# Kernel tuning notes

Measured on AMD Instinct MI355X. Metric: run time of the kernel, lower is better.

Reference implementation:

```python
import jax, jax.numpy as jnp
import numpy as np

N = 50000      # nodes
E = 800000     # edges (before self loops)
D_IN = 256
D_H = 256
D_OUT = 64     # num_classes
SLOPE = 0.01   # leaky_relu slope


def setup_inputs() -> dict:
    key = jax.random.key(0)
    ks = jax.random.split(key, 8)
    x = jax.random.normal(ks[0], (N, D_IN), dtype=jnp.float32)
    edge_index = jax.random.randint(ks[1], (2, E), 0, N, dtype=jnp.int32)
    s = 0.05
    W1 = jax.random.normal(ks[2], (D_H, D_IN), dtype=jnp.float32) * s
    b1 = jnp.zeros((D_H,), dtype=jnp.float32)
    W2 = jax.random.normal(ks[3], (D_H, D_H), dtype=jnp.float32) * s
    b2 = jnp.zeros((D_H,), dtype=jnp.float32)
    W3 = jax.random.normal(ks[4], (D_OUT, D_H), dtype=jnp.float32) * s
    b3 = jnp.zeros((D_OUT,), dtype=jnp.float32)
    return {"x": x, "edge_index": edge_index, "W1": W1, "b1": b1,
            "W2": W2, "b2": b2, "W3": W3, "b3": b3}


def _gcn_layer(x, W, b, src, dst):
    # PyG GCNConv: h = x @ W^T; out[dst] += d^{-1/2}[src] d^{-1/2}[dst] * h[src]; out += b
    h = x @ W.T                                             # [N, out]
    ones = jnp.ones(src.shape[0], dtype=h.dtype)
    deg = jax.ops.segment_sum(ones, dst, num_segments=N)    # includes self loops
    dinv = jnp.where(deg > 0, jax.lax.rsqrt(deg), 0.0)
    norm = dinv[src] * dinv[dst]                            # [E+N]
    msg = h[src] * norm[:, None]                            # gather + scale
    out = jax.ops.segment_sum(msg, dst, num_segments=N)     # scatter-add
    return out + b


def reference(x, edge_index, W1, b1, W2, b2, W3, b3):
    src, dst = edge_index[0], edge_index[1]
    loop = jnp.arange(N, dtype=src.dtype)                   # add self loops
    src = jnp.concatenate([src, loop])
    dst = jnp.concatenate([dst, loop])
    act = lambda h: jax.nn.leaky_relu(h, negative_slope=SLOPE)
    h1 = act(_gcn_layer(x, W1, b1, src, dst))
    h2 = act(_gcn_layer(h1, W2, b2, src, dst))
    logits = _gcn_layer(h2, W3, b3, src, dst)               # no activation on last layer
    return (h1, h2, logits)
```

## Files before the change

kernel.cpp:

```cpp
#include <hip/hip_runtime.h>

#define N_NODES 50000
#define E_EDGES 800000
#define SLOPE 0.01f

typedef __attribute__((ext_vector_type(8))) short bf16x8;
typedef __attribute__((ext_vector_type(4))) float floatx4;

__device__ __forceinline__ unsigned short f2bf(float f) {
    unsigned u = __builtin_bit_cast(unsigned, f);
    unsigned r = (u + 0x7FFFu + ((u >> 16) & 1u)) >> 16;
    return (unsigned short)r;
}
__device__ __forceinline__ float bf2f(unsigned short h) {
    unsigned u = ((unsigned)h) << 16;
    return __builtin_bit_cast(float, u);
}


__global__ void f32_to_bf16_kernel(const float* __restrict__ in,
                                   unsigned short* __restrict__ out, int n4) {
    int i = blockIdx.x * blockDim.x + threadIdx.x;
    if (i < n4) {
        float4 v = ((const float4*)in)[i];
        ushort4 o;
        o.x = f2bf(v.x); o.y = f2bf(v.y); o.z = f2bf(v.z); o.w = f2bf(v.w);
        ((ushort4*)out)[i] = o;
    }
}

__global__ void wfrag_kernel(const float* __restrict__ Wf,
                             unsigned short* __restrict__ out, int n4) {
    int idx = blockIdx.x * blockDim.x + threadIdx.x;
    if (idx >= n4) return;
    int n = idx >> 6;
    int k = (idx & 63) << 2;
    float4 v = ((const float4*)Wf)[idx];
    int jt = n >> 4, lm = n & 15, kk = k >> 5, q = (k >> 3) & 3, e = k & 7;
    int off = ((jt * 8 + kk) * 64 + q * 16 + lm) * 8 + e;
    ushort4 o;
    o.x = f2bf(v.x); o.y = f2bf(v.y); o.z = f2bf(v.z); o.w = f2bf(v.w);
    *(ushort4*)(out + off) = o;
}


__global__ void zero_counts_kernel(int* __restrict__ counts) {
    int i = blockIdx.x * blockDim.x + threadIdx.x;
    if (i < N_NODES) counts[i] = 0;
}

__global__ void hist_kernel(const int* __restrict__ dst, int* __restrict__ counts) {
    int e = blockIdx.x * blockDim.x + threadIdx.x;
    if (e < E_EDGES) atomicAdd(&counts[dst[e]], 1);
}

__global__ void dinv_kernel(const int* __restrict__ counts, float* __restrict__ dinv) {
    int i = blockIdx.x * blockDim.x + threadIdx.x;
    if (i < N_NODES) dinv[i] = rsqrtf((float)(counts[i] + 1));
}

#define SB 1024
__global__ __launch_bounds__(SB) void scan1_kernel(const int* __restrict__ counts,
                                                   int* __restrict__ partial,
                                                   int* __restrict__ bsum) {
    __shared__ int wsum[16];
    int tid = threadIdx.x, lane = tid & 63, wid = tid >> 6;
    int i = blockIdx.x * SB + tid;
    int v = (i < N_NODES) ? counts[i] : 0;
    int x = v;
    #pragma unroll
    for (int off = 1; off < 64; off <<= 1) {
        int y = __shfl_up(x, off, 64);
        if (lane >= off) x += y;
    }
    if (lane == 63) wsum[wid] = x;
    __syncthreads();
    if (wid == 0) {
        int s = (lane < 16) ? wsum[lane] : 0;
        #pragma unroll
        for (int off = 1; off < 16; off <<= 1) {
            int y = __shfl_up(s, off, 64);
            if (lane >= off) s += y;
        }
        if (lane < 16) wsum[lane] = s;
    }
    __syncthreads();
    int woff = wid ? wsum[wid - 1] : 0;
    if (i < N_NODES) partial[i] = woff + x - v;
    if (tid == SB - 1) bsum[blockIdx.x] = woff + x;
}

__global__ void scan2_kernel(int* __restrict__ bsum, int nb) {
    int lane = threadIdx.x;
    int v = (lane < nb) ? bsum[lane] : 0;
    #pragma unroll
    for (int off = 1; off < 64; off <<= 1) {
        int y = __shfl_up(v, off, 64);
        if (lane >= off) v += y;
    }
    if (lane < nb) bsum[lane] = v;
}

__global__ void scan3_kernel(int* __restrict__ row_ptr, const int* __restrict__ bsum,
                             int* __restrict__ cursor, int nb) {
    int i = blockIdx.x * blockDim.x + threadIdx.x;
    if (i < N_NODES) {
        int c = i >> 10;
        int off = c ? bsum[c - 1] : 0;
        int ex = row_ptr[i] + off;
        row_ptr[i] = ex;
        cursor[i] = ex;
    }
    if (i == 0) row_ptr[N_NODES] = bsum[nb - 1];
}

__global__ void scatter_kernel(const int* __restrict__ src, const int* __restrict__ dst,
                               int* __restrict__ cursor, int* __restrict__ col_idx) {
    int e = blockIdx.x * blockDim.x + threadIdx.x;
    if (e < E_EDGES) {
        int pos = atomicAdd(&cursor[dst[e]], 1);
        col_idx[pos] = src[e];
    }
}


template<int WAVES_M, int WAVES_N, int MT, int NT>
__global__ __launch_bounds__(256) void gemm_frag_kernel(
        const unsigned short* __restrict__ Ab,
        const unsigned short* __restrict__ Bf,
        const float* __restrict__ dinv,
        unsigned short* __restrict__ C, int M, int Nc) {
    const int wave = threadIdx.x >> 6, lane = threadIdx.x & 63;
    const int lm = lane & 15, q = lane >> 4;
    const int bm = blockIdx.x * (WAVES_M * MT * 16);
    const int bn = blockIdx.y * (WAVES_N * NT * 16);
    const int wm = (wave / WAVES_N) * (MT * 16);
    const int wn = (wave % WAVES_N) * (NT * 16);
    const int jt0 = (bn + wn) >> 4;

    const unsigned short* arow[MT];
    #pragma unroll
    for (int i = 0; i < MT; ++i) {
        int r = bm + wm + i * 16 + lm;
        if (r >= M) r = M - 1;
        arow[i] = Ab + (size_t)r * 256 + q * 8;
    }

    floatx4 acc[MT][NT] = {};

    #pragma unroll
    for (int kk = 0; kk < 8; ++kk) {
        bf16x8 a[MT], b[NT];
        #pragma unroll
        for (int i = 0; i < MT; ++i)
            a[i] = *(const bf16x8*)(arow[i] + kk * 32);
        #pragma unroll
        for (int j = 0; j < NT; ++j)
            b[j] = *(const bf16x8*)(Bf + (((jt0 + j) * 8 + kk) * 64 + lane) * 8);
        #pragma unroll
        for (int i = 0; i < MT; ++i)
            #pragma unroll
            for (int j = 0; j < NT; ++j)
                acc[i][j] = __builtin_amdgcn_mfma_f32_16x16x32_bf16(a[i], b[j], acc[i][j], 0, 0, 0);
    }

    #pragma unroll
    for (int i = 0; i < MT; ++i) {
        int rb = bm + wm + i * 16 + q * 4;
        #pragma unroll
        for (int r = 0; r < 4; ++r) {
            int row = rb + r;
            if (row < M) {
                float dd = dinv[row];
                #pragma unroll
                for (int j = 0; j < NT; ++j)
                    C[(size_t)row * Nc + bn + wn + j * 16 + lm] = f2bf(acc[i][j][r] * dd);
            }
        }
    }
}


template<bool ACT>
__global__ __launch_bounds__(256) void agg256_kernel(
        const int* __restrict__ row_ptr, const int* __restrict__ col_idx,
        const float* __restrict__ dinv, const unsigned short* __restrict__ hs,
        const float* __restrict__ bias,
        float* __restrict__ out, unsigned short* __restrict__ outb) {
    int node = __builtin_amdgcn_readfirstlane(blockIdx.x * 4 + (threadIdx.x >> 6));
    int lane = threadIdx.x & 63;

    float dd = dinv[node];
    ushort4 sv = ((const ushort4*)(hs + (size_t)node * 256))[lane];
    float ax = bf2f(sv.x), ay = bf2f(sv.y), az = bf2f(sv.z), aw = bf2f(sv.w);

    int beg = row_ptr[node], end = row_ptr[node + 1];
    int j = beg;
    for (; j + 3 < end; j += 4) {
        int s0 = col_idx[j], s1 = col_idx[j + 1], s2 = col_idx[j + 2], s3 = col_idx[j + 3];
        ushort4 v0 = ((const ushort4*)(hs + (size_t)s0 * 256))[lane];
        ushort4 v1 = ((const ushort4*)(hs + (size_t)s1 * 256))[lane];
        ushort4 v2 = ((const ushort4*)(hs + (size_t)s2 * 256))[lane];
        ushort4 v3 = ((const ushort4*)(hs + (size_t)s3 * 256))[lane];
        ax += bf2f(v0.x); ay += bf2f(v0.y); az += bf2f(v0.z); aw += bf2f(v0.w);
        ax += bf2f(v1.x); ay += bf2f(v1.y); az += bf2f(v1.z); aw += bf2f(v1.w);
        ax += bf2f(v2.x); ay += bf2f(v2.y); az += bf2f(v2.z); aw += bf2f(v2.w);
        ax += bf2f(v3.x); ay += bf2f(v3.y); az += bf2f(v3.z); aw += bf2f(v3.w);
    }
    for (; j < end; ++j) {
        int s = col_idx[j];
        ushort4 v = ((const ushort4*)(hs + (size_t)s * 256))[lane];
        ax += bf2f(v.x); ay += bf2f(v.y); az += bf2f(v.z); aw += bf2f(v.w);
    }

    const float4 b4 = ((const float4*)bias)[lane];
    ax = fmaf(ax, dd, b4.x); ay = fmaf(ay, dd, b4.y);
    az = fmaf(az, dd, b4.z); aw = fmaf(aw, dd, b4.w);
    if (ACT) {
        ax = ax > 0.f ? ax : SLOPE * ax;
        ay = ay > 0.f ? ay : SLOPE * ay;
        az = az > 0.f ? az : SLOPE * az;
        aw = aw > 0.f ? aw : SLOPE * aw;
    }
    float4 o; o.x = ax; o.y = ay; o.z = az; o.w = aw;
    ((float4*)(out + (size_t)node * 256))[lane] = o;
    ushort4 ob; ob.x = f2bf(ax); ob.y = f2bf(ay); ob.z = f2bf(az); ob.w = f2bf(aw);
    ((ushort4*)(outb + (size_t)node * 256))[lane] = ob;
}

__global__ __launch_bounds__(256) void agg64_kernel(
        const int* __restrict__ row_ptr, const int* __restrict__ col_idx,
        const float* __restrict__ dinv, const unsigned short* __restrict__ hs,
        const float* __restrict__ bias, float* __restrict__ out) {
    int node = __builtin_amdgcn_readfirstlane(blockIdx.x * 4 + (threadIdx.x >> 6));
    int lane = threadIdx.x & 63;

    float dd = dinv[node];
    float acc = bf2f(hs[(size_t)node * 64 + lane]);

    int beg = row_ptr[node], end = row_ptr[node + 1];
    int j = beg;
    for (; j + 3 < end; j += 4) {
        int s0 = col_idx[j], s1 = col_idx[j + 1], s2 = col_idx[j + 2], s3 = col_idx[j + 3];
        acc += bf2f(hs[(size_t)s0 * 64 + lane]);
        acc += bf2f(hs[(size_t)s1 * 64 + lane]);
        acc += bf2f(hs[(size_t)s2 * 64 + lane]);
        acc += bf2f(hs[(size_t)s3 * 64 + lane]);
    }
    for (; j < end; ++j)
        acc += bf2f(hs[(size_t)col_idx[j] * 64 + lane]);

    acc = fmaf(acc, dd, bias[lane]);
    out[(size_t)node * 64 + lane] = acc;
}


static inline int cdiv(long long a, long long b) { return (int)((a + b - 1) / b); }

extern "C" void kernel_launch(void* const* d_in, const int* in_sizes, int n_in,
                              void* d_out, int out_size, void* d_ws, size_t ws_size,
                              hipStream_t stream) {
    const float* x  = (const float*)d_in[0];
    const int* ei   = (const int*)d_in[1];
    const float* W1 = (const float*)d_in[2];
    const float* b1 = (const float*)d_in[3];
    const float* W2 = (const float*)d_in[4];
    const float* b2 = (const float*)d_in[5];
    const float* W3 = (const float*)d_in[6];
    const float* b3 = (const float*)d_in[7];

    const int* src = ei;
    const int* dst = ei + E_EDGES;

    char* ws = (char*)d_ws;
    int*   counts  = (int*)ws;   ws += 50048 * 4;
    int*   cursor  = (int*)ws;   ws += 50048 * 4;
    int*   row_ptr = (int*)ws;   ws += 50112 * 4;
    float* dinv    = (float*)ws; ws += 50048 * 4;
    int*   bsum    = (int*)ws;   ws += 64 * 4;
    int*   col_idx = (int*)ws;   ws += (size_t)E_EDGES * 4;
    unsigned short* W1f = (unsigned short*)ws; ws += 65536 * 2;
    unsigned short* W2f = (unsigned short*)ws; ws += 65536 * 2;
    unsigned short* W3f = (unsigned short*)ws; ws += 16384 * 2;
    unsigned short* hb  = (unsigned short*)ws; ws += (size_t)N_NODES * 256 * 2;
    unsigned short* ob  = (unsigned short*)ws;

    float* out1 = (float*)d_out;
    float* out2 = out1 + (size_t)N_NODES * 256;
    float* out3 = out2 + (size_t)N_NODES * 256;

    const int NB = cdiv(N_NODES, SB);

    f32_to_bf16_kernel<<<cdiv((long long)N_NODES * 256 / 4, 256), 256, 0, stream>>>(
        x, ob, N_NODES * 256 / 4);
    wfrag_kernel<<<cdiv(256 * 64, 256), 256, 0, stream>>>(W1, W1f, 256 * 64);
    wfrag_kernel<<<cdiv(256 * 64, 256), 256, 0, stream>>>(W2, W2f, 256 * 64);
    wfrag_kernel<<<cdiv(64 * 64, 256), 256, 0, stream>>>(W3, W3f, 64 * 64);

    zero_counts_kernel<<<cdiv(N_NODES, 256), 256, 0, stream>>>(counts);
    hist_kernel<<<cdiv(E_EDGES, 256), 256, 0, stream>>>(dst, counts);
    dinv_kernel<<<cdiv(N_NODES, 256), 256, 0, stream>>>(counts, dinv);
    scan1_kernel<<<NB, SB, 0, stream>>>(counts, row_ptr, bsum);
    scan2_kernel<<<1, 64, 0, stream>>>(bsum, NB);
    scan3_kernel<<<cdiv(N_NODES, 256), 256, 0, stream>>>(row_ptr, bsum, cursor, NB);
    scatter_kernel<<<cdiv(E_EDGES, 256), 256, 0, stream>>>(src, dst, cursor, col_idx);

    dim3 g256(cdiv(N_NODES, 128), 2);
    dim3 g64(cdiv(N_NODES, 256), 1);
    int agg_grid = cdiv(N_NODES, 4);

    gemm_frag_kernel<2, 2, 4, 4><<<g256, 256, 0, stream>>>(ob, W1f, dinv, hb, N_NODES, 256);
    agg256_kernel<true><<<agg_grid, 256, 0, stream>>>(row_ptr, col_idx, dinv, hb, b1, out1, ob);

    gemm_frag_kernel<2, 2, 4, 4><<<g256, 256, 0, stream>>>(ob, W2f, dinv, hb, N_NODES, 256);
    agg256_kernel<true><<<agg_grid, 256, 0, stream>>>(row_ptr, col_idx, dinv, hb, b2, out2, ob);

    gemm_frag_kernel<4, 1, 4, 4><<<g64, 256, 0, stream>>>(ob, W3f, dinv, hb, N_NODES, 64);
    agg64_kernel<<<agg_grid, 256, 0, stream>>>(row_ptr, col_idx, dinv, hb, b3, out3);
}
```

Before: 475.4 us.

## Fuse prep kernels, overlap CSR scatter with first GEMM, widen aggregation loads

Merges the histogram, input conversion and weight fragment kernels into one launch. It folds dinv into scan1 and scan2 into scan3, and runs the CSR scatter in the same grid as the first GEMM, so fewer launches are needed and independent work can overlap. The aggregation kernels now use 16-byte and 8-byte loads with half-waves or quarter-waves handling different edges, followed by a shuffle reduction. This raises memory-level parallelism at the cost of extra shuffles and a more complex lane remap.

```diff
diff --git a/kernel.cpp b/kernel.cpp
--- a/kernel.cpp
+++ b/kernel.cpp
@@ -16,11 +16,23 @@
     unsigned u = ((unsigned)h) << 16;
     return __builtin_bit_cast(float, u);
 }
-
-
-__global__ void f32_to_bf16_kernel(const float* __restrict__ in,
-                                   unsigned short* __restrict__ out, int n4) {
-    int i = blockIdx.x * blockDim.x + threadIdx.x;
+__device__ __forceinline__ float blo(unsigned u) { return __builtin_bit_cast(float, u << 16); }
+__device__ __forceinline__ float bhi(unsigned u) { return __builtin_bit_cast(float, u & 0xFFFF0000u); }
+
+__device__ __forceinline__ void acc8(uint4 v, float a[8]) {
+    a[0] += blo(v.x); a[1] += bhi(v.x);
+    a[2] += blo(v.y); a[3] += bhi(v.y);
+    a[4] += blo(v.z); a[5] += bhi(v.z);
+    a[6] += blo(v.w); a[7] += bhi(v.w);
+}
+__device__ __forceinline__ void acc4(uint2 v, float a[4]) {
+    a[0] += blo(v.x); a[1] += bhi(v.x);
+    a[2] += blo(v.y); a[3] += bhi(v.y);
+}
+
+
+__device__ __forceinline__ void conv_body(const float* __restrict__ in,
+                                          unsigned short* __restrict__ out, int i, int n4) {
     if (i < n4) {
         float4 v = ((const float4*)in)[i];
         ushort4 o;
@@ -29,9 +41,8 @@
     }
 }
 
-__global__ void wfrag_kernel(const float* __restrict__ Wf,
-                             unsigned short* __restrict__ out, int n4) {
-    int idx = blockIdx.x * blockDim.x + threadIdx.x;
+__device__ __forceinline__ void wfrag_body(const float* __restrict__ Wf,
+                                           unsigned short* __restrict__ out, int idx, int n4) {
     if (idx >= n4) return;
     int n = idx >> 6;
     int k = (idx & 63) << 2;
@@ -43,26 +54,40 @@
     *(ushort4*)(out + off) = o;
 }
 
-
-__global__ void zero_counts_kernel(int* __restrict__ counts) {
-    int i = blockIdx.x * blockDim.x + threadIdx.x;
-    if (i < N_NODES) counts[i] = 0;
-}
-
-__global__ void hist_kernel(const int* __restrict__ dst, int* __restrict__ counts) {
-    int e = blockIdx.x * blockDim.x + threadIdx.x;
-    if (e < E_EDGES) atomicAdd(&counts[dst[e]], 1);
-}
-
-__global__ void dinv_kernel(const int* __restrict__ counts, float* __restrict__ dinv) {
-    int i = blockIdx.x * blockDim.x + threadIdx.x;
-    if (i < N_NODES) dinv[i] = rsqrtf((float)(counts[i] + 1));
-}
+#define PREP_HIST_B   3125
+#define PREP_CONV_B   12500
+#define PREP_W1_B     64
+#define PREP_W2_B     64
+#define PREP_W3_B     16
+#define PREP_TOTAL_B  (PREP_HIST_B + PREP_CONV_B + PREP_W1_B + PREP_W2_B + PREP_W3_B)
+
+__global__ __launch_bounds__(256) void prep0_kernel(
+        const float* __restrict__ x, unsigned short* __restrict__ xb,
+        const float* __restrict__ W1, unsigned short* __restrict__ W1f,
+        const float* __restrict__ W2, unsigned short* __restrict__ W2f,
+        const float* __restrict__ W3, unsigned short* __restrict__ W3f,
+        const int* __restrict__ dst, int* __restrict__ counts) {
+    int b = blockIdx.x, tid = threadIdx.x;
+    if (b < PREP_HIST_B) {
+        int e = b * 256 + tid;
+        if (e < E_EDGES) atomicAdd(&counts[dst[e]], 1);
+    } else if (b < PREP_HIST_B + PREP_CONV_B) {
+        conv_body(x, xb, (b - PREP_HIST_B) * 256 + tid, N_NODES * 256 / 4);
+    } else if (b < PREP_HIST_B + PREP_CONV_B + PREP_W1_B) {
+        wfrag_body(W1, W1f, (b - PREP_HIST_B - PREP_CONV_B) * 256 + tid, 16384);
+    } else if (b < PREP_HIST_B + PREP_CONV_B + PREP_W1_B + PREP_W2_B) {
+        wfrag_body(W2, W2f, (b - PREP_HIST_B - PREP_CONV_B - PREP_W1_B) * 256 + tid, 16384);
+    } else {
+        wfrag_body(W3, W3f, (b - PREP_HIST_B - PREP_CONV_B - PREP_W1_B - PREP_W2_B) * 256 + tid, 4096);
+    }
+}
+
 
 #define SB 1024
-__global__ __launch_bounds__(SB) void scan1_kernel(const int* __restrict__ counts,
-                                                   int* __restrict__ partial,
-                                                   int* __restrict__ bsum) {
+__global__ __launch_bounds__(SB) void scan1_dinv_kernel(const int* __restrict__ counts,
+                                                        int* __restrict__ partial,
+                                                        int* __restrict__ bsum,
+                                                        float* __restrict__ dinv) {
     __shared__ int wsum[16];
     int tid = threadIdx.x, lane = tid & 63, wid = tid >> 6;
     int i = blockIdx.x * SB + tid;
@@ -86,54 +111,51 @@
     }
     __syncthreads();
     int woff = wid ? wsum[wid - 1] : 0;
-    if (i < N_NODES) partial[i] = woff + x - v;
+    if (i < N_NODES) {
+        partial[i] = woff + x - v;
+        dinv[i] = rsqrtf((float)(v + 1));
+    }
     if (tid == SB - 1) bsum[blockIdx.x] = woff + x;
 }
 
-__global__ void scan2_kernel(int* __restrict__ bsum, int nb) {
-    int lane = threadIdx.x;
-    int v = (lane < nb) ? bsum[lane] : 0;
-    #pragma unroll
-    for (int off = 1; off < 64; off <<= 1) {
-        int y = __shfl_up(v, off, 64);
-        if (lane >= off) v += y;
-    }
-    if (lane < nb) bsum[lane] = v;
-}
-
-__global__ void scan3_kernel(int* __restrict__ row_ptr, const int* __restrict__ bsum,
-                             int* __restrict__ cursor, int nb) {
-    int i = blockIdx.x * blockDim.x + threadIdx.x;
+__global__ __launch_bounds__(256) void scan3b_kernel(int* __restrict__ row_ptr,
+                                                     const int* __restrict__ bsum,
+                                                     int* __restrict__ cursor, int nb) {
+    __shared__ int pref[64];
+    int tid = threadIdx.x;
+    if (tid < 64) {
+        int v = (tid < nb) ? bsum[tid] : 0;
+        #pragma unroll
+        for (int off = 1; off < 64; off <<= 1) {
+            int y = __shfl_up(v, off, 64);
+            if (tid >= off) v += y;
+        }
+        pref[tid] = v;
+    }
+    __syncthreads();
+    int i = blockIdx.x * 256 + tid;
     if (i < N_NODES) {
         int c = i >> 10;
-        int off = c ? bsum[c - 1] : 0;
+        int off = c ? pref[c - 1] : 0;
         int ex = row_ptr[i] + off;
         row_ptr[i] = ex;
         cursor[i] = ex;
     }
-    if (i == 0) row_ptr[N_NODES] = bsum[nb - 1];
-}
-
-__global__ void scatter_kernel(const int* __restrict__ src, const int* __restrict__ dst,
-                               int* __restrict__ cursor, int* __restrict__ col_idx) {
-    int e = blockIdx.x * blockDim.x + threadIdx.x;
-    if (e < E_EDGES) {
-        int pos = atomicAdd(&cursor[dst[e]], 1);
-        col_idx[pos] = src[e];
-    }
+    if (i == 0) row_ptr[N_NODES] = pref[nb - 1];
 }
 
 
 template<int WAVES_M, int WAVES_N, int MT, int NT>
-__global__ __launch_bounds__(256) void gemm_frag_kernel(
+__device__ __forceinline__ void gemm_frag_body(
+        int bx, int by, int tid,
         const unsigned short* __restrict__ Ab,
         const unsigned short* __restrict__ Bf,
         const float* __restrict__ dinv,
         unsigned short* __restrict__ C, int M, int Nc) {
-    const int wave = threadIdx.x >> 6, lane = threadIdx.x & 63;
+    const int wave = tid >> 6, lane = tid & 63;
     const int lm = lane & 15, q = lane >> 4;
-    const int bm = blockIdx.x * (WAVES_M * MT * 16);
-    const int bn = blockIdx.y * (WAVES_N * NT * 16);
+    const int bm = bx * (WAVES_M * MT * 16);
+    const int bn = by * (WAVES_N * NT * 16);
     const int wm = (wave / WAVES_N) * (MT * 16);
     const int wn = (wave % WAVES_N) * (NT * 16);
     const int jt0 = (bn + wn) >> 4;
@@ -180,6 +202,36 @@
     }
 }
 
+__global__ __launch_bounds__(256) void gemm256_kernel(
+        const unsigned short* __restrict__ Ab, const unsigned short* __restrict__ Bf,
+        const float* __restrict__ dinv, unsigned short* __restrict__ C, int M, int Nc) {
+    gemm_frag_body<2, 2, 4, 4>(blockIdx.x, blockIdx.y, threadIdx.x, Ab, Bf, dinv, C, M, Nc);
+}
+
+__global__ __launch_bounds__(256) void gemm64_kernel(
+        const unsigned short* __restrict__ Ab, const unsigned short* __restrict__ Bf,
+        const float* __restrict__ dinv, unsigned short* __restrict__ C, int M, int Nc) {
+    gemm_frag_body<4, 1, 4, 4>(blockIdx.x, 0, threadIdx.x, Ab, Bf, dinv, C, M, Nc);
+}
+
+#define GEMM1_B 782
+__global__ __launch_bounds__(256) void gemm1_scatter_kernel(
+        const unsigned short* __restrict__ Ab, const unsigned short* __restrict__ Bf,
+        const float* __restrict__ dinv, unsigned short* __restrict__ C, int M, int Nc,
+        const int* __restrict__ src, const int* __restrict__ dst,
+        int* __restrict__ cursor, int* __restrict__ col_idx) {
+    int b = blockIdx.x;
+    if (b < GEMM1_B) {
+        gemm_frag_body<2, 2, 4, 4>(b >> 1, b & 1, threadIdx.x, Ab, Bf, dinv, C, M, Nc);
+    } else {
+        int e = (b - GEMM1_B) * 256 + threadIdx.x;
+        if (e < E_EDGES) {
+            int pos = atomicAdd(&cursor[dst[e]], 1);
+            col_idx[pos] = src[e];
+        }
+    }
+}
+
 
 template<bool ACT>
 __global__ __launch_bounds__(256) void agg256_kernel(
@@ -189,42 +241,61 @@
         float* __restrict__ out, unsigned short* __restrict__ outb) {
     int node = __builtin_amdgcn_readfirstlane(blockIdx.x * 4 + (threadIdx.x >> 6));
     int lane = threadIdx.x & 63;
-
-    float dd = dinv[node];
-    ushort4 sv = ((const ushort4*)(hs + (size_t)node * 256))[lane];
-    float ax = bf2f(sv.x), ay = bf2f(sv.y), az = bf2f(sv.z), aw = bf2f(sv.w);
+    int half = lane >> 5, sl = lane & 31;
+
+    float a[8] = {};
 
     int beg = row_ptr[node], end = row_ptr[node + 1];
     int j = beg;
-    for (; j + 3 < end; j += 4) {
-        int s0 = col_idx[j], s1 = col_idx[j + 1], s2 = col_idx[j + 2], s3 = col_idx[j + 3];
-        ushort4 v0 = ((const ushort4*)(hs + (size_t)s0 * 256))[lane];
-        ushort4 v1 = ((const ushort4*)(hs + (size_t)s1 * 256))[lane];
-        ushort4 v2 = ((const ushort4*)(hs + (size_t)s2 * 256))[lane];
-        ushort4 v3 = ((const ushort4*)(hs + (size_t)s3 * 256))[lane];
-        ax += bf2f(v0.x); ay += bf2f(v0.y); az += bf2f(v0.z); aw += bf2f(v0.w);
-        ax += bf2f(v1.x); ay += bf2f(v1.y); az += bf2f(v1.z); aw += bf2f(v1.w);
-        ax += bf2f(v2.x); ay += bf2f(v2.y); az += bf2f(v2.z); aw += bf2f(v2.w);
-        ax += bf2f(v3.x); ay += bf2f(v3.y); az += bf2f(v3.z); aw += bf2f(v3.w);
-    }
-    for (; j < end; ++j) {
+    for (; j + 8 <= end; j += 8) {
+        int s0 = col_idx[j + half];
+        int s1 = col_idx[j + 2 + half];
+        int s2 = col_idx[j + 4 + half];
+        int s3 = col_idx[j + 6 + half];
+        uint4 v0 = ((const uint4*)(hs + (size_t)s0 * 256))[sl];
+        uint4 v1 = ((const uint4*)(hs + (size_t)s1 * 256))[sl];
+        uint4 v2 = ((const uint4*)(hs + (size_t)s2 * 256))[sl];
+        uint4 v3 = ((const uint4*)(hs + (size_t)s3 * 256))[sl];
+        acc8(v0, a); acc8(v1, a); acc8(v2, a); acc8(v3, a);
+    }
+    for (; j + 2 <= end; j += 2) {
+        int s = col_idx[j + half];
+        uint4 v = ((const uint4*)(hs + (size_t)s * 256))[sl];
+        acc8(v, a);
+    }
+    if (j < end && half == 0) {
         int s = col_idx[j];
-        ushort4 v = ((const ushort4*)(hs + (size_t)s * 256))[lane];
-        ax += bf2f(v.x); ay += bf2f(v.y); az += bf2f(v.z); aw += bf2f(v.w);
-    }
-
+        uint4 v = ((const uint4*)(hs + (size_t)s * 256))[sl];
+        acc8(v, a);
+    }
+
+    #pragma unroll
+    for (int k = 0; k < 8; ++k) a[k] += __shfl_xor(a[k], 32);
+
+    uint4 sv = ((const uint4*)(hs + (size_t)node * 256))[sl];
+    acc8(sv, a);
+
+    int srcl = lane >> 1;
+    float t0 = __shfl(a[0], srcl), t1 = __shfl(a[1], srcl);
+    float t2 = __shfl(a[2], srcl), t3 = __shfl(a[3], srcl);
+    float t4 = __shfl(a[4], srcl), t5 = __shfl(a[5], srcl);
+    float t6 = __shfl(a[6], srcl), t7 = __shfl(a[7], srcl);
+    bool hi = (lane & 1);
+    float f0 = hi ? t4 : t0, f1 = hi ? t5 : t1, f2 = hi ? t6 : t2, f3 = hi ? t7 : t3;
+
+    float dd = dinv[node];
     const float4 b4 = ((const float4*)bias)[lane];
-    ax = fmaf(ax, dd, b4.x); ay = fmaf(ay, dd, b4.y);
-    az = fmaf(az, dd, b4.z); aw = fmaf(aw, dd, b4.w);
+    f0 = fmaf(f0, dd, b4.x); f1 = fmaf(f1, dd, b4.y);
+    f2 = fmaf(f2, dd, b4.z); f3 = fmaf(f3, dd, b4.w);
     if (ACT) {
-        ax = ax > 0.f ? ax : SLOPE * ax;
-        ay = ay > 0.f ? ay : SLOPE * ay;
-        az = az > 0.f ? az : SLOPE * az;
-        aw = aw > 0.f ? aw : SLOPE * aw;
-    }
-    float4 o; o.x = ax; o.y = ay; o.z = az; o.w = aw;
+        f0 = f0 > 0.f ? f0 : SLOPE * f0;
+        f1 = f1 > 0.f ? f1 : SLOPE * f1;
+        f2 = f2 > 0.f ? f2 : SLOPE * f2;
+        f3 = f3 > 0.f ? f3 : SLOPE * f3;
+    }
+    float4 o; o.x = f0; o.y = f1; o.z = f2; o.w = f3;
     ((float4*)(out + (size_t)node * 256))[lane] = o;
-    ushort4 ob; ob.x = f2bf(ax); ob.y = f2bf(ay); ob.z = f2bf(az); ob.w = f2bf(aw);
+    ushort4 ob; ob.x = f2bf(f0); ob.y = f2bf(f1); ob.z = f2bf(f2); ob.w = f2bf(f3);
     ((ushort4*)(outb + (size_t)node * 256))[lane] = ob;
 }
 
@@ -234,24 +305,49 @@
         const float* __restrict__ bias, float* __restrict__ out) {
     int node = __builtin_amdgcn_readfirstlane(blockIdx.x * 4 + (threadIdx.x >> 6));
     int lane = threadIdx.x & 63;
-
-    float dd = dinv[node];
-    float acc = bf2f(hs[(size_t)node * 64 + lane]);
+    int g = lane >> 4, sl = lane & 15;
+
+    float a[4] = {};
 
     int beg = row_ptr[node], end = row_ptr[node + 1];
     int j = beg;
-    for (; j + 3 < end; j += 4) {
-        int s0 = col_idx[j], s1 = col_idx[j + 1], s2 = col_idx[j + 2], s3 = col_idx[j + 3];
-        acc += bf2f(hs[(size_t)s0 * 64 + lane]);
-        acc += bf2f(hs[(size_t)s1 * 64 + lane]);
-        acc += bf2f(hs[(size_t)s2 * 64 + lane]);
-        acc += bf2f(hs[(size_t)s3 * 64 + lane]);
-    }
-    for (; j < end; ++j)
-        acc += bf2f(hs[(size_t)col_idx[j] * 64 + lane]);
-
-    acc = fmaf(acc, dd, bias[lane]);
-    out[(size_t)node * 64 + lane] = acc;
+    for (; j + 8 <= end; j += 8) {
+        int s0 = col_idx[j + g];
+        int s1 = col_idx[j + 4 + g];
+        uint2 v0 = ((const uint2*)(hs + (size_t)s0 * 64))[sl];
+        uint2 v1 = ((const uint2*)(hs + (size_t)s1 * 64))[sl];
+        acc4(v0, a); acc4(v1, a);
+    }
+    for (; j + 4 <= end; j += 4) {
+        int s = col_idx[j + g];
+        uint2 v = ((const uint2*)(hs + (size_t)s * 64))[sl];
+        acc4(v, a);
+    }
+    int rem = end - j;
+    if (g < rem) {
+        int s = col_idx[j + g];
+        uint2 v = ((const uint2*)(hs + (size_t)s * 64))[sl];
+        acc4(v, a);
+    }
+
+    #pragma unroll
+    for (int k = 0; k < 4; ++k) {
+        a[k] += __shfl_xor(a[k], 16);
+        a[k] += __shfl_xor(a[k], 32);
+    }
+
+    uint2 sv = ((const uint2*)(hs + (size_t)node * 64))[sl];
+    acc4(sv, a);
+
+    float dd = dinv[node];
+    const float4 b4 = ((const float4*)bias)[sl];
+    float4 o;
+    o.x = fmaf(a[0], dd, b4.x);
+    o.y = fmaf(a[1], dd, b4.y);
+    o.z = fmaf(a[2], dd, b4.z);
+    o.w = fmaf(a[3], dd, b4.w);
+    if (g == 0)
+        ((float4*)(out + (size_t)node * 64))[sl] = o;
 }
 
 
@@ -291,30 +387,23 @@
 
     const int NB = cdiv(N_NODES, SB);
 
-    f32_to_bf16_kernel<<<cdiv((long long)N_NODES * 256 / 4, 256), 256, 0, stream>>>(
-        x, ob, N_NODES * 256 / 4);
-    wfrag_kernel<<<cdiv(256 * 64, 256), 256, 0, stream>>>(W1, W1f, 256 * 64);
-    wfrag_kernel<<<cdiv(256 * 64, 256), 256, 0, stream>>>(W2, W2f, 256 * 64);
-    wfrag_kernel<<<cdiv(64 * 64, 256), 256, 0, stream>>>(W3, W3f, 64 * 64);
-
-    zero_counts_kernel<<<cdiv(N_NODES, 256), 256, 0, stream>>>(counts);
-    hist_kernel<<<cdiv(E_EDGES, 256), 256, 0, stream>>>(dst, counts);
-    dinv_kernel<<<cdiv(N_NODES, 256), 256, 0, stream>>>(counts, dinv);
-    scan1_kernel<<<NB, SB, 0, stream>>>(counts, row_ptr, bsum);
-    scan2_kernel<<<1, 64, 0, stream>>>(bsum, NB);
-    scan3_kernel<<<cdiv(N_NODES, 256), 256, 0, stream>>>(row_ptr, bsum, cursor, NB);
-    scatter_kernel<<<cdiv(E_EDGES, 256), 256, 0, stream>>>(src, dst, cursor, col_idx);
+    hipMemsetAsync(counts, 0, 50048 * sizeof(int), stream);
+    prep0_kernel<<<PREP_TOTAL_B, 256, 0, stream>>>(x, ob, W1, W1f, W2, W2f, W3, W3f, dst, counts);
+
+    scan1_dinv_kernel<<<NB, SB, 0, stream>>>(counts, row_ptr, bsum, dinv);
+    scan3b_kernel<<<cdiv(N_NODES, 256), 256, 0, stream>>>(row_ptr, bsum, cursor, NB);
 
     dim3 g256(cdiv(N_NODES, 128), 2);
     dim3 g64(cdiv(N_NODES, 256), 1);
     int agg_grid = cdiv(N_NODES, 4);
 
-    gemm_frag_kernel<2, 2, 4, 4><<<g256, 256, 0, stream>>>(ob, W1f, dinv, hb, N_NODES, 256);
+    gemm1_scatter_kernel<<<GEMM1_B + PREP_HIST_B, 256, 0, stream>>>(
+        ob, W1f, dinv, hb, N_NODES, 256, src, dst, cursor, col_idx);
     agg256_kernel<true><<<agg_grid, 256, 0, stream>>>(row_ptr, col_idx, dinv, hb, b1, out1, ob);
 
-    gemm_frag_kernel<2, 2, 4, 4><<<g256, 256, 0, stream>>>(ob, W2f, dinv, hb, N_NODES, 256);
+    gemm256_kernel<<<g256, 256, 0, stream>>>(ob, W2f, dinv, hb, N_NODES, 256);
     agg256_kernel<true><<<agg_grid, 256, 0, stream>>>(row_ptr, col_idx, dinv, hb, b2, out2, ob);
 
-    gemm_frag_kernel<4, 1, 4, 4><<<g64, 256, 0, stream>>>(ob, W3f, dinv, hb, N_NODES, 64);
+    gemm64_kernel<<<g64, 256, 0, stream>>>(ob, W3f, dinv, hb, N_NODES, 64);
     agg64_kernel<<<agg_grid, 256, 0, stream>>>(row_ptr, col_idx, dinv, hb, b3, out3);
 }
```

Result: faster. 449.8 us (-5.4%).
